# Kernel tuning notes

Measured on AMD Instinct MI355X. Metric: run time of the kernel, lower is better.

Reference implementation:

```python
import jax, jax.numpy as jnp
import numpy as np

N_NODES = 50000


def gcn_conv(x, src, dst, W, b, num_nodes):
    """PyG GCNConv: y = D^{-1/2} (A + I) D^{-1/2} (x @ W) + b.
    src/dst already include self-loops."""
    h = x @ W  # [N, F_out]
    deg = jax.ops.segment_sum(jnp.ones_like(dst, dtype=h.dtype), dst,
                              num_segments=num_nodes)  # in-degree incl. self-loop
    dinv = jnp.where(deg > 0, jax.lax.rsqrt(deg), 0.0)
    norm = dinv[src] * dinv[dst]  # [E]
    msgs = h[src] * norm[:, None]  # gather + scale, [E, F_out]
    out = jax.ops.segment_sum(msgs, dst, num_segments=num_nodes)
    return out + b


def setup_inputs() -> dict:
    key = jax.random.key(0)
    k1, k2, k3, k4 = jax.random.split(key, 4)
    latent, hidden, out_ch = 64, 128, 64
    n_edges = 800000
    z = jax.random.normal(k1, (N_NODES, latent), dtype=jnp.float32)
    edge_index = jax.random.randint(k2, (2, n_edges), 0, N_NODES, dtype=jnp.int64)
    # Glorot-style scaled weights
    W1 = jax.random.normal(k3, (latent, hidden), dtype=jnp.float32) * (1.0 / np.sqrt(latent))
    b1 = jnp.zeros((hidden,), dtype=jnp.float32)
    W2 = jax.random.normal(k4, (hidden, out_ch), dtype=jnp.float32) * (1.0 / np.sqrt(hidden))
    b2 = jnp.zeros((out_ch,), dtype=jnp.float32)
    return {"z": z, "edge_index": edge_index, "W1": W1, "b1": b1, "W2": W2, "b2": b2}


def reference(z, edge_index, W1, b1, W2, b2):
    num_nodes = z.shape[0]
    loops = jnp.arange(num_nodes, dtype=edge_index.dtype)
    src = jnp.concatenate([edge_index[0], loops])  # add self-loops
    dst = jnp.concatenate([edge_index[1], loops])
    x = gcn_conv(z, src, dst, W1, b1, num_nodes)
    x = jax.nn.relu(x)
    x = gcn_conv(x, src, dst, W2, b2, num_nodes)
    x = jax.nn.relu(x)
    return x
```

## Files before the change

### kernel.cpp

```cpp
#include <hip/hip_runtime.h>
#include <hip/hip_fp16.h>

static inline size_t align256(size_t x){ return (x + 255) & ~(size_t)255; }

#define CAP 64
#define NPART 8

__device__ __forceinline__ int detect_is64(const unsigned* __restrict__ e){
  unsigned v = e[2 * (threadIdx.x & 63) + 1];
  return (__ballot(v != 0u) == 0ull) ? 1 : 0;
}
__device__ __forceinline__ int load_idx(const void* edges, long i, int is64){
  return is64 ? (int)((const long long*)edges)[i] : ((const int*)edges)[i];
}

__device__ __forceinline__ float fdot2u(unsigned a, unsigned b, float c){
#if defined(__has_builtin) && __has_builtin(__builtin_amdgcn_fdot2)
  typedef _Float16 h2 __attribute__((ext_vector_type(2)));
  return __builtin_amdgcn_fdot2(__builtin_bit_cast(h2, a),
                                __builtin_bit_cast(h2, b), c, false);
#else
  const float2 fa = __half22float2(*(const __half2*)&a);
  const float2 fb = __half22float2(*(const __half2*)&b);
  return fmaf(fa.y, fb.y, fmaf(fa.x, fb.x, c));
#endif
}

__global__ __launch_bounds__(256) void pack_kernel(const void* __restrict__ edges, int E,
                                                   unsigned* __restrict__ pe,
                                                   int* __restrict__ cnt, int N){
  const int is64 = detect_is64((const unsigned*)edges);
  const int t0 = blockIdx.x * 256 + threadIdx.x;
  const int stride = gridDim.x * 256;
  for (int i = t0; i < N; i += stride) cnt[i] = 0;
  for (int i = t0; i < E; i += stride){
    const unsigned s = (unsigned)load_idx(edges, i, is64);
    const unsigned d = (unsigned)load_idx(edges, (long)E + i, is64);
    pe[i] = (d << 16) | (s & 0xFFFFu);
  }
}

__global__ __launch_bounds__(256) void build_kernel(const unsigned* __restrict__ pe, int E,
                                                    int* __restrict__ cnt,
                                                    unsigned short* __restrict__ csr,
                                                    int N){
  const int p  = blockIdx.x & (NPART - 1);
  const int q  = blockIdx.x >> 3;
  const int nq = gridDim.x >> 3;
  const int nper = (N + NPART - 1) / NPART;
  const int lo = p * nper;
  const int hi = min(lo + nper, N);
  const int stride = nq * 256;
  for (int i = q * 256 + threadIdx.x; i < E; i += stride){
    const unsigned v = pe[i];
    const int d = (int)(v >> 16);
    if (d < lo || d >= hi) continue;
    const int pos = atomicAdd(&cnt[d], 1);
    if (pos < CAP) csr[((size_t)d << 6) + pos] = (unsigned short)(v & 0xFFFFu);
  }
}

__device__ __forceinline__ void h8_acc(uint4 r, float* a){
  const __half2* h = (const __half2*)&r;
  #pragma unroll
  for (int k = 0; k < 4; ++k){
    const float2 f = __half22float2(h[k]);
    a[2*k]     += f.x;
    a[2*k + 1] += f.y;
  }
}

__device__ __forceinline__ void gather8(const uint4* __restrict__ H,
                                        const unsigned short* __restrict__ row,
                                        int deg, int j, float* a){
  int e = 0;
  #pragma unroll 1
  for (; e + 4 <= deg; e += 4){
    const ushort4 rr = *(const ushort4*)(row + e);
    const uint4 v0 = H[(size_t)rr.x * 8 + j];
    const uint4 v1 = H[(size_t)rr.y * 8 + j];
    const uint4 v2 = H[(size_t)rr.z * 8 + j];
    const uint4 v3 = H[(size_t)rr.w * 8 + j];
    h8_acc(v0, a); h8_acc(v1, a); h8_acc(v2, a); h8_acc(v3, a);
  }
  #pragma unroll 1
  for (; e < deg; ++e) h8_acc(H[(size_t)row[e] * 8 + j], a);
}

__global__ __launch_bounds__(256) void prep_kernel(const float4* __restrict__ z,
                                                   uint4* __restrict__ zh,
                                                   const int* __restrict__ cnt,
                                                   float* __restrict__ dinv, int N){
  const int idx = blockIdx.x * 256 + threadIdx.x;
  const int node = idx >> 3;
  if (node >= N) return;
  const int j = idx & 7;
  const float di = rsqrtf((float)(cnt[node] + 1));
  if (j == 0) dinv[node] = di;
  const float4 v0 = z[(size_t)node * 16 + j * 2];
  const float4 v1 = z[(size_t)node * 16 + j * 2 + 1];
  const __half2 a0 = __float22half2_rn(make_float2(di * v0.x, di * v0.y));
  const __half2 a1 = __float22half2_rn(make_float2(di * v0.z, di * v0.w));
  const __half2 a2 = __float22half2_rn(make_float2(di * v1.x, di * v1.y));
  const __half2 a3 = __float22half2_rn(make_float2(di * v1.z, di * v1.w));
  uint4 r;
  r.x = *(const unsigned*)&a0; r.y = *(const unsigned*)&a1;
  r.z = *(const unsigned*)&a2; r.w = *(const unsigned*)&a3;
  zh[idx] = r;
}

__global__ __launch_bounds__(512) void fused1_kernel(const uint4* __restrict__ zh,
                                                     const unsigned short* __restrict__ csr,
                                                     const int* __restrict__ cnt,
                                                     const float* __restrict__ dinv,
                                                     const float* __restrict__ W1,
                                                     const float* __restrict__ b1,
                                                     const float* __restrict__ W2,
                                                     __half* __restrict__ h2, int N){
  __shared__ unsigned wl[4096];
  __shared__ unsigned rows2[2048];
  __shared__ unsigned x1t[4096];
  const int t = threadIdx.x;

  {
    #pragma unroll
    for (int c = 0; c < 8; ++c){
      const int idx = t + c * 512;
      const int k2 = idx >> 7, jc = idx & 127;
      const float w0 = W1[(2 * k2) * 128 + jc];
      const float w1 = W1[(2 * k2 + 1) * 128 + jc];
      const __half2 hh = __float22half2_rn(make_float2(w0, w1));
      wl[idx] = *(const unsigned*)&hh;
    }
  }

  const int local = t >> 3;
  const int j = t & 7;
  const int node = blockIdx.x * 64 + local;
  float a[8] = {0.f, 0.f, 0.f, 0.f, 0.f, 0.f, 0.f, 0.f};
  float di = 0.f;
  if (node < N){
    di = dinv[node];
    h8_acc(zh[(size_t)node * 8 + j], a);
    const int deg = min(cnt[node], CAP);
    gather8(zh, csr + ((size_t)node << 6), deg, j, a);
  }
  #pragma unroll
  for (int m = 0; m < 4; ++m){
    const __half2 hh = __float22half2_rn(make_float2(a[2*m] * di, a[2*m+1] * di));
    const int k2 = (j * 4 + m) ^ (local & 31);
    rows2[local * 32 + k2] = *(const unsigned*)&hh;
  }
  __syncthreads();

  const int jc = t & 127;
  const int g = t >> 7;
  {
    const float bv = b1[jc];
    float accv[16];
    #pragma unroll
    for (int n = 0; n < 16; ++n) accv[n] = bv;

    #pragma unroll 4
    for (int k2 = 0; k2 < 32; ++k2){
      const unsigned w = wl[k2 * 128 + jc];
      #pragma unroll
      for (int n = 0; n < 16; ++n){
        const int nn = g * 16 + n;
        accv[n] = fdot2u(rows2[nn * 32 + (k2 ^ (nn & 31))], w, accv[n]);
      }
    }
    unsigned short* x1h = (unsigned short*)x1t;
    #pragma unroll
    for (int n = 0; n < 16; ++n){
      const int nn = g * 16 + n;
      const __half hv = __float2half(fmaxf(accv[n], 0.0f));
      const int u = nn * 64 + ((jc >> 1) ^ ((nn & 7) << 3));
      x1h[u * 2 + (jc & 1)] = *(const unsigned short*)&hv;
    }
  }
  __syncthreads();

  {
    #pragma unroll
    for (int c = 0; c < 8; ++c){
      const int idx = t + c * 512;
      const int k2 = idx >> 6, jc2 = idx & 63;
      const float w0 = W2[(2 * k2) * 64 + jc2];
      const float w1 = W2[(2 * k2 + 1) * 64 + jc2];
      const __half2 hh = __float22half2_rn(make_float2(w0, w1));
      wl[idx] = *(const unsigned*)&hh;
    }
  }
  __syncthreads();

  const int cg = t & 15;
  const int ng = t >> 4;
  const int n0 = ng * 2, n1 = n0 + 1;
  float acc0[4] = {0.f,0.f,0.f,0.f}, acc1[4] = {0.f,0.f,0.f,0.f};
  #pragma unroll 4
  for (int k2 = 0; k2 < 64; ++k2){
    const unsigned xa = x1t[n0 * 64 + (k2 ^ ((n0 & 7) << 3))];
    const unsigned xb = x1t[n1 * 64 + (k2 ^ ((n1 & 7) << 3))];
    const uint4 wv = *(const uint4*)&wl[k2 * 64 + cg * 4];
    acc0[0] = fdot2u(xa, wv.x, acc0[0]);
    acc0[1] = fdot2u(xa, wv.y, acc0[1]);
    acc0[2] = fdot2u(xa, wv.z, acc0[2]);
    acc0[3] = fdot2u(xa, wv.w, acc0[3]);
    acc1[0] = fdot2u(xb, wv.x, acc1[0]);
    acc1[1] = fdot2u(xb, wv.y, acc1[1]);
    acc1[2] = fdot2u(xb, wv.z, acc1[2]);
    acc1[3] = fdot2u(xb, wv.w, acc1[3]);
  }
  const int gn0 = blockIdx.x * 64 + n0;
  const int gn1 = gn0 + 1;
  if (gn0 < N){
    const float d0 = dinv[gn0];
    const __half2 h0 = __float22half2_rn(make_float2(acc0[0]*d0, acc0[1]*d0));
    const __half2 h1 = __float22half2_rn(make_float2(acc0[2]*d0, acc0[3]*d0));
    uint2 r; r.x = *(const unsigned*)&h0; r.y = *(const unsigned*)&h1;
    *(uint2*)&h2[(size_t)gn0 * 64 + cg * 4] = r;
  }
  if (gn1 < N){
    const float d1 = dinv[gn1];
    const __half2 h0 = __float22half2_rn(make_float2(acc1[0]*d1, acc1[1]*d1));
    const __half2 h1 = __float22half2_rn(make_float2(acc1[2]*d1, acc1[3]*d1));
    uint2 r; r.x = *(const unsigned*)&h0; r.y = *(const unsigned*)&h1;
    *(uint2*)&h2[(size_t)gn1 * 64 + cg * 4] = r;
  }
}

__global__ __launch_bounds__(256) void agg2_kernel(const uint4* __restrict__ X,
                                                   float4* __restrict__ Y,
                                                   const unsigned short* __restrict__ csr,
                                                   const int* __restrict__ cnt,
                                                   const float* __restrict__ dinv,
                                                   const float4* __restrict__ bias,
                                                   int N){
  const int local = threadIdx.x >> 3;
  const int j = threadIdx.x & 7;
  const int node = blockIdx.x * 32 + local;
  if (node >= N) return;
  float a[8] = {0.f, 0.f, 0.f, 0.f, 0.f, 0.f, 0.f, 0.f};
  h8_acc(X[(size_t)node * 8 + j], a);
  const int deg = min(cnt[node], CAP);
  gather8(X, csr + ((size_t)node << 6), deg, j, a);
  const float di = dinv[node];
  const float4 b0 = bias[j * 2];
  const float4 b1v = bias[j * 2 + 1];
  float4 o0, o1;
  o0.x = fmaxf(fmaf(di, a[0], b0.x), 0.f);
  o0.y = fmaxf(fmaf(di, a[1], b0.y), 0.f);
  o0.z = fmaxf(fmaf(di, a[2], b0.z), 0.f);
  o0.w = fmaxf(fmaf(di, a[3], b0.w), 0.f);
  o1.x = fmaxf(fmaf(di, a[4], b1v.x), 0.f);
  o1.y = fmaxf(fmaf(di, a[5], b1v.y), 0.f);
  o1.z = fmaxf(fmaf(di, a[6], b1v.z), 0.f);
  o1.w = fmaxf(fmaf(di, a[7], b1v.w), 0.f);
  Y[(size_t)node * 16 + j * 2] = o0;
  Y[(size_t)node * 16 + j * 2 + 1] = o1;
}

extern "C" void kernel_launch(void* const* d_in, const int* in_sizes, int n_in,
                              void* d_out, int out_size, void* d_ws, size_t ws_size,
                              hipStream_t stream){
  const float* z  = (const float*)d_in[0];
  const void*  edges = d_in[1];
  const float* W1 = (const float*)d_in[2];
  const float* b1 = (const float*)d_in[3];
  const float* W2 = (const float*)d_in[4];
  const float* b2 = (const float*)d_in[5];
  float* out = (float*)d_out;

  constexpr int F0 = 64;
  const int N = in_sizes[0] / F0;
  const int E = in_sizes[1] / 2;
  (void)n_in; (void)out_size;

  char* p = (char*)d_ws;
  int*            cnt  = (int*)p;            p += align256((size_t)N * 4);
  float*          dinv = (float*)p;          p += align256((size_t)N * 4);
  unsigned short* csr  = (unsigned short*)p; p += align256((size_t)N * CAP * 2);
  unsigned*       pe   = (unsigned*)p;       p += align256((size_t)E * 4);
  __half*         zh   = (__half*)p;         p += align256((size_t)N * F0 * 2);
  __half*         h2   = (__half*)p;         p += align256((size_t)N * F0 * 2);
  (void)ws_size;

  pack_kernel<<<1024, 256, 0, stream>>>(edges, E, pe, cnt, N);
  build_kernel<<<1024, 256, 0, stream>>>(pe, E, cnt, csr, N);
  prep_kernel<<<(N * 8 + 255) / 256, 256, 0, stream>>>(
      (const float4*)z, (uint4*)zh, cnt, dinv, N);

  fused1_kernel<<<(N + 63) / 64, 512, 0, stream>>>(
      (const uint4*)zh, csr, cnt, dinv, W1, b1, W2, h2, N);

  agg2_kernel<<<(N + 31) / 32, 256, 0, stream>>>(
      (const uint4*)h2, (float4*)out, csr, cnt, dinv, (const float4*)b2, N);
}
```

Measured before the change: 191.4 us.

## Accumulate gathered neighbors in packed half and vectorize LDS matmul loads

The neighbor gather now sums up to 16 neighbor rows with packed half2 adds before converting to float. This cuts conversion and FP32 add work at the cost of fp16 accumulation error. The layer-1 and layer-2 shared-memory matmuls now read rows with 128-bit LDS loads in place of scalar swizzled reads, using a new swizzle at 4-word granularity to limit bank conflicts. The aim is fewer LDS instructions and less ALU overhead per FMA.

```diff
diff --git a/kernel.cpp b/kernel.cpp
--- a/kernel.cpp
+++ b/kernel.cpp
@@ -70,18 +70,31 @@
   }
 }
 
+__device__ __forceinline__ uint4 pkadd4(uint4 x, uint4 y){
+  __half2* a = (__half2*)&x;
+  const __half2* b = (const __half2*)&y;
+  a[0] = __hadd2(a[0], b[0]); a[1] = __hadd2(a[1], b[1]);
+  a[2] = __hadd2(a[2], b[2]); a[3] = __hadd2(a[3], b[3]);
+  return x;
+}
+
 __device__ __forceinline__ void gather8(const uint4* __restrict__ H,
                                         const unsigned short* __restrict__ row,
                                         int deg, int j, float* a){
   int e = 0;
-  #pragma unroll 1
-  for (; e + 4 <= deg; e += 4){
-    const ushort4 rr = *(const ushort4*)(row + e);
-    const uint4 v0 = H[(size_t)rr.x * 8 + j];
-    const uint4 v1 = H[(size_t)rr.y * 8 + j];
-    const uint4 v2 = H[(size_t)rr.z * 8 + j];
-    const uint4 v3 = H[(size_t)rr.w * 8 + j];
-    h8_acc(v0, a); h8_acc(v1, a); h8_acc(v2, a); h8_acc(v3, a);
+  while (e + 4 <= deg){
+    uint4 hs = make_uint4(0u, 0u, 0u, 0u);
+    const int lim = min(deg, e + 16);
+    #pragma unroll 1
+    for (; e + 4 <= lim; e += 4){
+      const ushort4 rr = *(const ushort4*)(row + e);
+      const uint4 v0 = H[(size_t)rr.x * 8 + j];
+      const uint4 v1 = H[(size_t)rr.y * 8 + j];
+      const uint4 v2 = H[(size_t)rr.z * 8 + j];
+      const uint4 v3 = H[(size_t)rr.w * 8 + j];
+      hs = pkadd4(hs, pkadd4(pkadd4(v0, v1), pkadd4(v2, v3)));
+    }
+    h8_acc(hs, a);
   }
   #pragma unroll 1
   for (; e < deg; ++e) h8_acc(H[(size_t)row[e] * 8 + j], a);
@@ -145,11 +158,15 @@
     const int deg = min(cnt[node], CAP);
     gather8(zh, csr + ((size_t)node << 6), deg, j, a);
   }
-  #pragma unroll
-  for (int m = 0; m < 4; ++m){
-    const __half2 hh = __float22half2_rn(make_float2(a[2*m] * di, a[2*m+1] * di));
-    const int k2 = (j * 4 + m) ^ (local & 31);
-    rows2[local * 32 + k2] = *(const unsigned*)&hh;
+  {
+    uint4 hh;
+    const __half2 p0 = __float22half2_rn(make_float2(a[0]*di, a[1]*di));
+    const __half2 p1 = __float22half2_rn(make_float2(a[2]*di, a[3]*di));
+    const __half2 p2 = __float22half2_rn(make_float2(a[4]*di, a[5]*di));
+    const __half2 p3 = __float22half2_rn(make_float2(a[6]*di, a[7]*di));
+    hh.x = *(const unsigned*)&p0; hh.y = *(const unsigned*)&p1;
+    hh.z = *(const unsigned*)&p2; hh.w = *(const unsigned*)&p3;
+    *(uint4*)&rows2[local * 32 + j * 4] = hh;
   }
   __syncthreads();
 
@@ -161,22 +178,37 @@
     #pragma unroll
     for (int n = 0; n < 16; ++n) accv[n] = bv;
 
-    #pragma unroll 4
-    for (int k2 = 0; k2 < 32; ++k2){
-      const unsigned w = wl[k2 * 128 + jc];
+    #pragma unroll
+    for (int c4 = 0; c4 < 4; ++c4){
+      unsigned wr[8];
+      #pragma unroll
+      for (int i = 0; i < 8; ++i) wr[i] = wl[(c4 * 8 + i) * 128 + jc];
       #pragma unroll
       for (int n = 0; n < 16; ++n){
         const int nn = g * 16 + n;
-        accv[n] = fdot2u(rows2[nn * 32 + (k2 ^ (nn & 31))], w, accv[n]);
+        const uint4 rA = *(const uint4*)&rows2[nn * 32 + c4 * 8];
+        const uint4 rB = *(const uint4*)&rows2[nn * 32 + c4 * 8 + 4];
+        const unsigned* ra = (const unsigned*)&rA;
+        const unsigned* rb = (const unsigned*)&rB;
+        accv[n] = fdot2u(ra[0], wr[0], accv[n]);
+        accv[n] = fdot2u(ra[1], wr[1], accv[n]);
+        accv[n] = fdot2u(ra[2], wr[2], accv[n]);
+        accv[n] = fdot2u(ra[3], wr[3], accv[n]);
+        accv[n] = fdot2u(rb[0], wr[4], accv[n]);
+        accv[n] = fdot2u(rb[1], wr[5], accv[n]);
+        accv[n] = fdot2u(rb[2], wr[6], accv[n]);
+        accv[n] = fdot2u(rb[3], wr[7], accv[n]);
       }
     }
     unsigned short* x1h = (unsigned short*)x1t;
+    const int k2o = jc >> 1;
+    const int kb = k2o >> 2, d = k2o & 3;
     #pragma unroll
     for (int n = 0; n < 16; ++n){
       const int nn = g * 16 + n;
       const __half hv = __float2half(fmaxf(accv[n], 0.0f));
-      const int u = nn * 64 + ((jc >> 1) ^ ((nn & 7) << 3));
-      x1h[u * 2 + (jc & 1)] = *(const unsigned short*)&hv;
+      const int word = nn * 64 + ((kb ^ ((nn & 3) << 2)) << 2) + d;
+      x1h[word * 2 + (jc & 1)] = *(const unsigned short*)&hv;
     }
   }
   __syncthreads();
@@ -199,18 +231,23 @@
   const int n0 = ng * 2, n1 = n0 + 1;
   float acc0[4] = {0.f,0.f,0.f,0.f}, acc1[4] = {0.f,0.f,0.f,0.f};
   #pragma unroll 4
-  for (int k2 = 0; k2 < 64; ++k2){
-    const unsigned xa = x1t[n0 * 64 + (k2 ^ ((n0 & 7) << 3))];
-    const unsigned xb = x1t[n1 * 64 + (k2 ^ ((n1 & 7) << 3))];
-    const uint4 wv = *(const uint4*)&wl[k2 * 64 + cg * 4];
-    acc0[0] = fdot2u(xa, wv.x, acc0[0]);
-    acc0[1] = fdot2u(xa, wv.y, acc0[1]);
-    acc0[2] = fdot2u(xa, wv.z, acc0[2]);
-    acc0[3] = fdot2u(xa, wv.w, acc0[3]);
-    acc1[0] = fdot2u(xb, wv.x, acc1[0]);
-    acc1[1] = fdot2u(xb, wv.y, acc1[1]);
-    acc1[2] = fdot2u(xb, wv.z, acc1[2]);
-    acc1[3] = fdot2u(xb, wv.w, acc1[3]);
+  for (int kb = 0; kb < 16; ++kb){
+    const uint4 xa4 = *(const uint4*)&x1t[n0 * 64 + ((kb ^ ((n0 & 3) << 2)) << 2)];
+    const uint4 xb4 = *(const uint4*)&x1t[n1 * 64 + ((kb ^ ((n1 & 3) << 2)) << 2)];
+    const unsigned* xav = (const unsigned*)&xa4;
+    const unsigned* xbv = (const unsigned*)&xb4;
+    #pragma unroll
+    for (int d = 0; d < 4; ++d){
+      const uint4 wv = *(const uint4*)&wl[(kb * 4 + d) * 64 + cg * 4];
+      acc0[0] = fdot2u(xav[d], wv.x, acc0[0]);
+      acc0[1] = fdot2u(xav[d], wv.y, acc0[1]);
+      acc0[2] = fdot2u(xav[d], wv.z, acc0[2]);
+      acc0[3] = fdot2u(xav[d], wv.w, acc0[3]);
+      acc1[0] = fdot2u(xbv[d], wv.x, acc1[0]);
+      acc1[1] = fdot2u(xbv[d], wv.y, acc1[1]);
+      acc1[2] = fdot2u(xbv[d], wv.z, acc1[2]);
+      acc1[3] = fdot2u(xbv[d], wv.w, acc1[3]);
+    }
   }
   const int gn0 = blockIdx.x * 64 + n0;
   const int gn1 = gn0 + 1;
```

Measured after the change: 170.4 us. 11.0% less time.
